# Optimization experiments

Measured on AMD Instinct MI355X. Metric: run time of the kernel, lower is better.

Reference implementation:

```python
import jax, jax.numpy as jnp
import numpy as np

HEAD_NUM = 8


def setup_inputs() -> dict:
    key = jax.random.key(0)
    ks = jax.random.split(key, 12)
    B, H, W, D = 8, 32, 32, 256
    Dh = D  # depth is even -> D_h = depth
    inner = Dh * HEAD_NUM
    s = 0.02
    inp = {
        "x": jax.random.normal(ks[0], (B, H, W, D), jnp.float32),
        "Kw": jax.random.normal(ks[1], (D, inner), jnp.float32) * s,
        "Kb": jnp.zeros((inner,), jnp.float32),
        "Qw": jax.random.normal(ks[2], (D, inner), jnp.float32) * s,
        "Qb": jnp.zeros((inner,), jnp.float32),
        "Vw": jax.random.normal(ks[3], (D, inner), jnp.float32) * s,
        "Vb": jnp.zeros((inner,), jnp.float32),
        "Pw": jax.random.normal(ks[4], (inner, D), jnp.float32) * s,
        "Pb": jnp.zeros((D,), jnp.float32),
        "row_tab": jax.random.normal(ks[5], (2 * H - 1, Dh // 2), jnp.float32) * s,
        "col_tab": jax.random.normal(ks[6], (2 * W - 1, Dh // 2), jnp.float32) * s,
    }
    return inp


def reference(x, Kw, Kb, Qw, Qb, Vw, Vb, Pw, Pb, row_tab, col_tab):
    B, H, W, D = x.shape
    hn = HEAD_NUM
    Dh = Kw.shape[1] // hn
    half = Dh // 2

    K = (x @ Kw + Kb).reshape(B, H, W, hn, Dh)
    Q = (x @ Qw + Qb).reshape(B, H, W, hn, Dh)
    V = (x @ Vw + Vb).reshape(B, H, W, hn, Dh)

    # content-content logits: [B,H,W,hn,H,W]
    score = jnp.einsum('bijhd,bklhd->bijhkl', Q, K)

    # relative row/col position bias via learned embeddings
    row_mat = jnp.arange(H)[None, :] - jnp.arange(H)[:, None] + H - 1  # (H,H)
    col_mat = jnp.arange(W)[:, None] - jnp.arange(W)[None, :] + W - 1  # (W,W)
    row_emb = row_tab[row_mat]  # (H,H,half)
    col_emb = col_tab[col_mat]  # (W,W,half)
    row_score = jnp.einsum('bijhd,ikd->bijhk', Q[..., :half], row_emb)[..., :, None]
    col_score = jnp.einsum('bijhd,jkd->bijhk', Q[..., half:], col_emb)[..., None, :]
    score = score + row_score + col_score

    attn = jax.nn.softmax(score.reshape(B, H, W, hn, H * W), axis=-1)
    attn = attn.reshape(B, H, W, hn, H, W)

    attended = jnp.einsum('bijhkl,bklhd->bijhd', attn, V).reshape(B, H, W, hn * Dh)
    return attended @ Pw + Pb
```

## Files before the change

kernel.cpp:

```cpp
#include <hip/hip_runtime.h>

typedef __attribute__((ext_vector_type(8))) short short8;
typedef __attribute__((ext_vector_type(4))) float f32x4;
typedef __attribute__((ext_vector_type(2))) unsigned int u32x2;
typedef __attribute__((ext_vector_type(4))) unsigned int u32x4;

__device__ __forceinline__ unsigned short f2bf(float f) {
  unsigned u = __float_as_uint(f);
  u += 0x7FFF + ((u >> 16) & 1);
  return (unsigned short)(u >> 16);
}
__device__ __forceinline__ unsigned packbf(float a, float b) {
  return (unsigned)f2bf(a) | ((unsigned)f2bf(b) << 16);
}
__device__ __forceinline__ float bf2f(unsigned short s) {
  return __uint_as_float(((unsigned)s) << 16);
}
__device__ __forceinline__ f32x4 mfma16(short8 a, short8 b, f32x4 c) {
  return __builtin_amdgcn_mfma_f32_16x16x32_bf16(a, b, c, 0, 0, 0);
}

typedef __attribute__((address_space(3))) unsigned int lds_u32;
typedef __attribute__((address_space(1))) const unsigned int glb_u32;
__device__ __forceinline__ void gll16(const void* g, void* l) {
  __builtin_amdgcn_global_load_lds((glb_u32*)g, (lds_u32*)l, 16, 0, 0);
}

__global__ void cvt_x_kernel(const float* __restrict__ in, unsigned short* __restrict__ out, int n) {
  int i = blockIdx.x * 256 + threadIdx.x;
  if (i < n) out[i] = f2bf(in[i]);
}

__global__ void transpose_cvt_kernel(const float* __restrict__ in, unsigned short* __restrict__ out,
                                     int K, int N) {
  int i = blockIdx.x * 256 + threadIdx.x;
  if (i < K * N) {
    int n = i / K, k = i - n * K;
    out[i] = f2bf(in[(size_t)k * N + n]);
  }
}

template<int MODE, int BMI>
__global__ __launch_bounds__(256, 2) void gemm128(const unsigned short* __restrict__ A,
    const unsigned short* __restrict__ BT, const float* __restrict__ bias,
    void* __restrict__ Cout, int Mdim, int Ndim, int Kdim) {
  constexpr int BM = 64 * BMI, MI = 2 * BMI;
  __shared__ short As[BM * 40];
  __shared__ short Bs[128 * 40];
  const int tid = threadIdx.x;
  const int wid = tid >> 6, lane = tid & 63;
  const int l15 = lane & 15, lg = lane >> 4;
  const int m0 = blockIdx.y * BM, n0 = blockIdx.x * 128;
  const int wr = (wid >> 1) * (BM / 2), wc = (wid & 1) * 64;
  const f32x4 z = {0.f, 0.f, 0.f, 0.f};
  f32x4 acc[MI][4];
#pragma unroll
  for (int mi = 0; mi < MI; ++mi)
#pragma unroll
    for (int ni = 0; ni < 4; ++ni) acc[mi][ni] = z;

  for (int kt = 0; kt < Kdim; kt += 32) {
#pragma unroll
    for (int it = 0; it < BMI; ++it) {
      int c = tid + it * 256;
      int row = c >> 2, c8 = (c & 3) * 8;
      *(short8*)&As[row * 40 + c8] = *(const short8*)(A + (size_t)(m0 + row) * Kdim + kt + c8);
    }
#pragma unroll
    for (int it = 0; it < 2; ++it) {
      int c = tid + it * 256;
      int row = c >> 2, c8 = (c & 3) * 8;
      *(short8*)&Bs[row * 40 + c8] = *(const short8*)(BT + (size_t)(n0 + row) * Kdim + kt + c8);
    }
    __syncthreads();
    short8 a[MI], b[4];
#pragma unroll
    for (int mi = 0; mi < MI; ++mi) a[mi] = *(const short8*)&As[(wr + mi * 16 + l15) * 40 + lg * 8];
#pragma unroll
    for (int ni = 0; ni < 4; ++ni) b[ni] = *(const short8*)&Bs[(wc + ni * 16 + l15) * 40 + lg * 8];
#pragma unroll
    for (int mi = 0; mi < MI; ++mi)
#pragma unroll
      for (int ni = 0; ni < 4; ++ni)
        acc[mi][ni] = mfma16(a[mi], b[ni], acc[mi][ni]);
    __syncthreads();
  }
#pragma unroll
  for (int mi = 0; mi < MI; ++mi)
#pragma unroll
    for (int ni = 0; ni < 4; ++ni)
#pragma unroll
      for (int e = 0; e < 4; ++e) {
        int gm = m0 + wr + mi * 16 + lg * 4 + e;
        int gn = n0 + wc + ni * 16 + l15;
        float v = acc[mi][ni][e] + bias[gn];
        if (MODE == 0) {
          ((unsigned short*)Cout)[(size_t)gm * Ndim + gn] = f2bf(v);
        } else if (MODE == 1) {
          ((float*)Cout)[(size_t)gm * Ndim + gn] = v;
        } else {
          int b_ = gm >> 10, pos = gm & 1023;
          int h = gn >> 8, d = gn & 255;
          ((unsigned short*)Cout)[((size_t)((b_ * 8 + h) * 256 + d)) * 1024 + pos] = f2bf(v);
        }
      }
}

__global__ __launch_bounds__(256, 4) void bias_mfma_kernel(const unsigned short* __restrict__ Q,
    const float* __restrict__ row_tab, const float* __restrict__ col_tab,
    float* __restrict__ Rb, float* __restrict__ Cb) {
  const int side = blockIdx.y >> 5;
  const int ij = blockIdx.y & 31;
  const int q4 = blockIdx.x;
  const int tid = threadIdx.x, wv = tid >> 6, lane = tid & 63;
  const int l15 = lane & 15, lg = lane >> 4;
  const float* tab = side ? col_tab : row_tab;
  const int doff = side ? 128 : 0;
  float* outp = side ? Cb : Rb;

  short8 eb[2][4];
#pragma unroll
  for (int nf = 0; nf < 2; ++nf) {
    int k = nf * 16 + l15;
    int trow = side ? (ij - k + 31) : (k - ij + 31);
    const float* tp = tab + (size_t)trow * 128 + lg * 8;
#pragma unroll
    for (int ks = 0; ks < 4; ++ks) {
      float4 f0 = *(const float4*)(tp + ks * 32);
      float4 f1 = *(const float4*)(tp + ks * 32 + 4);
      u32x4 r;
      r.x = packbf(f0.x, f0.y);
      r.y = packbf(f0.z, f0.w);
      r.z = packbf(f1.x, f1.y);
      r.w = packbf(f1.z, f1.w);
      eb[nf][ks] = *(short8*)&r;
    }
  }

  const f32x4 z = {0.f, 0.f, 0.f, 0.f};
  const int rbase = q4 * 512 + wv * 128;
#pragma unroll
  for (int mf = 0; mf < 8; ++mf) {
    int r = rbase + mf * 16 + l15;
    int b = r >> 8, jj = (r >> 3) & 31, h = r & 7;
    int q = side ? (jj * 32 + ij) : (ij * 32 + jj);
    const unsigned short* ap = Q + (size_t)(b * 1024 + q) * 2048 + h * 256 + doff + lg * 8;
    short8 af[4];
#pragma unroll
    for (int ks = 0; ks < 4; ++ks) af[ks] = *(const short8*)(ap + ks * 32);
    f32x4 a0 = z, a1 = z;
#pragma unroll
    for (int ks = 0; ks < 4; ++ks) {
      a0 = mfma16(af[ks], eb[0][ks], a0);
      a1 = mfma16(af[ks], eb[1][ks], a1);
    }
#pragma unroll
    for (int e = 0; e < 4; ++e) {
      int r2 = rbase + mf * 16 + lg * 4 + e;
      int b2 = r2 >> 8, jj2 = (r2 >> 3) & 31, h2 = r2 & 7;
      int q2 = side ? (jj2 * 32 + ij) : (ij * 32 + jj2);
      float* op = outp + ((size_t)((b2 * 8 + h2) * 1024 + q2)) * 32 + l15;
      op[0] = a0[e];
      op[16] = a1[e];
    }
  }
}

__global__ __launch_bounds__(512, 2) void attn_kernel(const unsigned short* __restrict__ Q,
    const unsigned short* __restrict__ K, const unsigned short* __restrict__ Vt,
    const float* __restrict__ Rb, const float* __restrict__ Cb,
    unsigned short* __restrict__ Att) {
  __shared__ __align__(16) char KV[4][32768];
  __shared__ unsigned short RbL[256 * 32];
  const int wgid = blockIdx.x;
  const int bh = (wgid & 7) * 8 + ((wgid >> 3) & 7);
  const int qblk = wgid >> 6;
  const int b = bh >> 3, h = bh & 7;
  const int tid = threadIdx.x, wv = tid >> 6, lane = tid & 63;
  const int l15 = lane & 15, lg = lane >> 4;
  const int q0w = qblk * 256 + wv * 32;

  const unsigned short* kbase = K + (size_t)(b * 1024) * 2048 + h * 256;
  const unsigned short* vbase = Vt + (size_t)bh * 256 * 1024;

  auto stage = [&](int buf, int t) {
#pragma unroll
    for (int it = 0; it < 2; ++it) {
      int s = it * 8192 + wv * 1024 + lane * 16;
      int key = s >> 9;
      int c = ((s >> 4) & 31) ^ (key & 7);
      gll16(kbase + (size_t)(t * 32 + key) * 2048 + c * 8, &KV[buf][it * 8192 + wv * 1024]);
    }
#pragma unroll
    for (int it = 0; it < 2; ++it) {
      int s = it * 8192 + wv * 1024 + lane * 16;
      int r = s >> 9;
      int cc = ((s >> 4) & 31) ^ (r & 7);
      int d = r * 8 + (cc >> 2);
      gll16(vbase + (size_t)d * 1024 + t * 32 + (cc & 3) * 8,
            &KV[buf][16384 + it * 8192 + wv * 1024]);
    }
  };

  stage(0, 0);
  stage(1, 1);

  short8 qa[2][8];
#pragma unroll
  for (int qf = 0; qf < 2; ++qf) {
    const unsigned short* qp = Q + (size_t)(b * 1024 + q0w + qf * 16 + l15) * 2048 + h * 256;
#pragma unroll
    for (int kk = 0; kk < 8; ++kk) qa[qf][kk] = *(const short8*)(qp + kk * 32 + lg * 8);
  }
  float4 cpre[2][2];
#pragma unroll
  for (int qf = 0; qf < 2; ++qf) {
    const float* cbp = Cb + ((size_t)bh * 1024 + q0w + qf * 16 + l15) * 32;
    cpre[qf][0] = *(const float4*)(cbp + lg * 4);
    cpre[qf][1] = *(const float4*)(cbp + 16 + lg * 4);
  }
  {
    const float* rsrc = Rb + ((size_t)bh * 1024 + qblk * 256) * 32;
#pragma unroll
    for (int i = 0; i < 16; ++i) {
      int idx = i * 512 + tid;
      RbL[idx] = f2bf(rsrc[idx]);
    }
  }
  asm volatile("s_waitcnt lgkmcnt(0)" ::: "memory");

  const f32x4 z = {0.f, 0.f, 0.f, 0.f};
  f32x4 o[16][2];
#pragma unroll
  for (int nf2 = 0; nf2 < 16; ++nf2) { o[nf2][0] = z; o[nf2][1] = z; }
  float m_r[2] = {-1e30f, -1e30f}, l_r[2] = {0.f, 0.f};

  const int nfd = lg >> 1;
  const int srcA = ((lg & 1) * 2) * 16 + l15, srcB = srcA + 16;
  const unsigned short* rbl0 = &RbL[(wv * 32 + l15) * 32];
  const unsigned short* rbl1 = rbl0 + 16 * 32;

  for (int t = 0; t < 32; ++t) {
    if (t < 30) stage((t + 2) & 3, t + 2);
    if (t < 30)       asm volatile("s_waitcnt vmcnt(8)" ::: "memory");
    else if (t == 30) asm volatile("s_waitcnt vmcnt(4)" ::: "memory");
    else              asm volatile("s_waitcnt vmcnt(0)" ::: "memory");
    __builtin_amdgcn_s_barrier();
    asm volatile("" ::: "memory");

    const char* kb = &KV[t & 3][0];
    const char* vb = &KV[t & 3][16384];

    f32x4 s[2][2] = {{z, z}, {z, z}};
#pragma unroll
    for (int kk = 0; kk < 8; ++kk) {
      int c0 = (kk * 4 + lg) ^ (l15 & 7);
      short8 k0 = *(const short8*)(kb + l15 * 512 + c0 * 16);
      int key1 = 16 + l15;
      int c1 = (kk * 4 + lg) ^ (key1 & 7);
      short8 k1 = *(const short8*)(kb + key1 * 512 + c1 * 16);
      s[0][0] = mfma16(k0, qa[0][kk], s[0][0]);
      s[1][0] = mfma16(k0, qa[1][kk], s[1][0]);
      s[0][1] = mfma16(k1, qa[0][kk], s[0][1]);
      s[1][1] = mfma16(k1, qa[1][kk], s[1][1]);
    }
    float rb0 = bf2f(rbl0[t]), rb1 = bf2f(rbl1[t]);
#pragma unroll
    for (int nf = 0; nf < 2; ++nf)
#pragma unroll
      for (int e = 0; e < 4; ++e) {
        s[0][nf][e] += rb0 + ((const float*)&cpre[0][nf])[e];
        s[1][nf][e] += rb1 + ((const float*)&cpre[1][nf])[e];
      }
    float tm[2];
#pragma unroll
    for (int qf = 0; qf < 2; ++qf) {
      float m2 = fmaxf(fmaxf(s[qf][0][0], s[qf][0][1]), fmaxf(s[qf][0][2], s[qf][0][3]));
#pragma unroll
      for (int e = 0; e < 4; ++e) m2 = fmaxf(m2, s[qf][1][e]);
      m2 = fmaxf(m2, __shfl_xor(m2, 16));
      m2 = fmaxf(m2, __shfl_xor(m2, 32));
      tm[qf] = m2;
    }
    if (__any((tm[0] > m_r[0] + 8.f) || (tm[1] > m_r[1] + 8.f))) {
#pragma unroll
      for (int qf = 0; qf < 2; ++qf) {
        float mn = fmaxf(m_r[qf], tm[qf]);
        float sc = __expf(m_r[qf] - mn);
        m_r[qf] = mn;
        l_r[qf] *= sc;
#pragma unroll
        for (int nf2 = 0; nf2 < 16; ++nf2)
#pragma unroll
          for (int e = 0; e < 4; ++e) o[nf2][qf][e] *= sc;
      }
    }
    short8 pb[2];
#pragma unroll
    for (int qf = 0; qf < 2; ++qf) {
      float ps = 0.f;
#pragma unroll
      for (int nf = 0; nf < 2; ++nf)
#pragma unroll
        for (int e = 0; e < 4; ++e) {
          float pv = __expf(s[qf][nf][e] - m_r[qf]);
          s[qf][nf][e] = pv;
          ps += pv;
        }
      ps += __shfl_xor(ps, 16);
      ps += __shfl_xor(ps, 32);
      l_r[qf] += ps;
      unsigned u0 = packbf(s[qf][0][0], s[qf][0][1]);
      unsigned u1 = packbf(s[qf][0][2], s[qf][0][3]);
      unsigned u2 = packbf(s[qf][1][0], s[qf][1][1]);
      unsigned u3 = packbf(s[qf][1][2], s[qf][1][3]);
      unsigned a0 = __shfl(u0, srcA), b0 = __shfl(u2, srcA);
      unsigned a1 = __shfl(u1, srcA), b1 = __shfl(u3, srcA);
      unsigned a2 = __shfl(u0, srcB), b2 = __shfl(u2, srcB);
      unsigned a3 = __shfl(u1, srcB), b3 = __shfl(u3, srcB);
      u32x4 r4;
      r4.x = nfd ? b0 : a0;
      r4.y = nfd ? b1 : a1;
      r4.z = nfd ? b2 : a2;
      r4.w = nfd ? b3 : a3;
      pb[qf] = *(short8*)&r4;
    }
#pragma unroll
    for (int nf2 = 0; nf2 < 16; ++nf2) {
      int d = nf2 * 16 + l15;
      int r = d >> 3;
      int cc = ((d & 7) * 4 + lg) ^ (r & 7);
      short8 vf = *(const short8*)(vb + r * 512 + cc * 16);
      o[nf2][0] = mfma16(vf, pb[0], o[nf2][0]);
      o[nf2][1] = mfma16(vf, pb[1], o[nf2][1]);
    }
  }
#pragma unroll
  for (int qf = 0; qf < 2; ++qf) {
    unsigned short* op = Att + (size_t)(b * 1024 + q0w + qf * 16 + l15) * 2048 + h * 256;
    float inv = 1.f / l_r[qf];
#pragma unroll
    for (int nf2 = 0; nf2 < 16; ++nf2) {
      u32x2 w;
      w.x = packbf(o[nf2][qf][0] * inv, o[nf2][qf][1] * inv);
      w.y = packbf(o[nf2][qf][2] * inv, o[nf2][qf][3] * inv);
      *(u32x2*)(op + nf2 * 16 + lg * 4) = w;
    }
  }
}

extern "C" void kernel_launch(void* const* d_in, const int* in_sizes, int n_in,
                              void* d_out, int out_size, void* d_ws, size_t ws_size,
                              hipStream_t stream) {
  (void)in_sizes; (void)n_in; (void)out_size;
  const float* x   = (const float*)d_in[0];
  const float* Kw  = (const float*)d_in[1];
  const float* Kb  = (const float*)d_in[2];
  const float* Qw  = (const float*)d_in[3];
  const float* Qb  = (const float*)d_in[4];
  const float* Vw  = (const float*)d_in[5];
  const float* Vb  = (const float*)d_in[6];
  const float* Pw  = (const float*)d_in[7];
  const float* Pb  = (const float*)d_in[8];
  const float* row_tab = (const float*)d_in[9];
  const float* col_tab = (const float*)d_in[10];
  float* out = (float*)d_out;

  char* ws = (char*)d_ws;
  size_t off = 0;
  auto alloc = [&](size_t bytes) { char* p = ws + off; off += bytes; return p; };
  unsigned short* Xb   = (unsigned short*)alloc((size_t)8192 * 256 * 2);
  unsigned short* WqT  = (unsigned short*)alloc((size_t)2048 * 256 * 2);
  unsigned short* WkT  = (unsigned short*)alloc((size_t)2048 * 256 * 2);
  unsigned short* WvT  = (unsigned short*)alloc((size_t)2048 * 256 * 2);
  unsigned short* PwT  = (unsigned short*)alloc((size_t)256 * 2048 * 2);
  unsigned short* Qg   = (unsigned short*)alloc((size_t)8192 * 2048 * 2);
  unsigned short* Kg   = (unsigned short*)alloc((size_t)8192 * 2048 * 2);
  unsigned short* VtG  = (unsigned short*)alloc((size_t)8192 * 2048 * 2);
  unsigned short* AttG = (unsigned short*)alloc((size_t)8192 * 2048 * 2);
  float* Rb = (float*)alloc((size_t)64 * 1024 * 32 * 4);
  float* Cb = (float*)alloc((size_t)64 * 1024 * 32 * 4);
  if (off > ws_size) return;

  cvt_x_kernel<<<8192, 256, 0, stream>>>(x, Xb, 8192 * 256);
  transpose_cvt_kernel<<<2048, 256, 0, stream>>>(Qw, WqT, 256, 2048);
  transpose_cvt_kernel<<<2048, 256, 0, stream>>>(Kw, WkT, 256, 2048);
  transpose_cvt_kernel<<<2048, 256, 0, stream>>>(Vw, WvT, 256, 2048);
  transpose_cvt_kernel<<<2048, 256, 0, stream>>>(Pw, PwT, 2048, 256);

  gemm128<0, 2><<<dim3(16, 64), 256, 0, stream>>>(Xb, WqT, Qb, Qg, 8192, 2048, 256);
  gemm128<0, 2><<<dim3(16, 64), 256, 0, stream>>>(Xb, WkT, Kb, Kg, 8192, 2048, 256);
  gemm128<2, 2><<<dim3(16, 64), 256, 0, stream>>>(Xb, WvT, Vb, VtG, 8192, 2048, 256);

  bias_mfma_kernel<<<dim3(4, 64), 256, 0, stream>>>(Qg, row_tab, col_tab, Rb, Cb);
  attn_kernel<<<256, 512, 0, stream>>>(Qg, Kg, VtG, Rb, Cb, AttG);
  gemm128<1, 1><<<dim3(2, 128), 256, 0, stream>>>(AttG, PwT, Pb, out, 8192, 256, 2048);
}
```

Before: 288.6 us.

## Halve attention workgroup size, double-buffer KV, compute softmax row sums via MFMA

The attention kernel now launches 512 workgroups of 256 threads, each covering 128 queries instead of 256, with a two-slot KV ring instead of four. A trailing barrier is added so a buffer is not overwritten while still being read. The softmax denominator is no longer reduced with shuffles; it is accumulated by an extra MFMA of a ones vector against the probability fragment. The RbL layout is transposed so each step reads a contiguous row. The goal is to raise occupancy and cut shuffle work, at the cost of a shallower prefetch pipeline, an extra barrier per step, and more redundant K/V loads across workgroups.

New measurement: 419.9 us. 1.46x slower.

```diff
diff --git a/kernel.cpp b/kernel.cpp
--- a/kernel.cpp
+++ b/kernel.cpp
@@ -166,44 +166,43 @@
   }
 }
 
-__global__ __launch_bounds__(512, 2) void attn_kernel(const unsigned short* __restrict__ Q,
+__global__ __launch_bounds__(256, 2) void attn_kernel(const unsigned short* __restrict__ Q,
     const unsigned short* __restrict__ K, const unsigned short* __restrict__ Vt,
     const float* __restrict__ Rb, const float* __restrict__ Cb,
     unsigned short* __restrict__ Att) {
-  __shared__ __align__(16) char KV[4][32768];
-  __shared__ unsigned short RbL[256 * 32];
+  __shared__ __align__(16) char KV[2][32768];
+  __shared__ unsigned short RbL[32 * 128];
   const int wgid = blockIdx.x;
   const int bh = (wgid & 7) * 8 + ((wgid >> 3) & 7);
   const int qblk = wgid >> 6;
   const int b = bh >> 3, h = bh & 7;
   const int tid = threadIdx.x, wv = tid >> 6, lane = tid & 63;
   const int l15 = lane & 15, lg = lane >> 4;
-  const int q0w = qblk * 256 + wv * 32;
+  const int q0w = qblk * 128 + wv * 32;
 
   const unsigned short* kbase = K + (size_t)(b * 1024) * 2048 + h * 256;
   const unsigned short* vbase = Vt + (size_t)bh * 256 * 1024;
 
   auto stage = [&](int buf, int t) {
 #pragma unroll
-    for (int it = 0; it < 2; ++it) {
-      int s = it * 8192 + wv * 1024 + lane * 16;
+    for (int it = 0; it < 4; ++it) {
+      int s = it * 4096 + wv * 1024 + lane * 16;
       int key = s >> 9;
       int c = ((s >> 4) & 31) ^ (key & 7);
-      gll16(kbase + (size_t)(t * 32 + key) * 2048 + c * 8, &KV[buf][it * 8192 + wv * 1024]);
-    }
-#pragma unroll
-    for (int it = 0; it < 2; ++it) {
-      int s = it * 8192 + wv * 1024 + lane * 16;
+      gll16(kbase + (size_t)(t * 32 + key) * 2048 + c * 8, &KV[buf][it * 4096 + wv * 1024]);
+    }
+#pragma unroll
+    for (int it = 0; it < 4; ++it) {
+      int s = it * 4096 + wv * 1024 + lane * 16;
       int r = s >> 9;
       int cc = ((s >> 4) & 31) ^ (r & 7);
       int d = r * 8 + (cc >> 2);
       gll16(vbase + (size_t)d * 1024 + t * 32 + (cc & 3) * 8,
-            &KV[buf][16384 + it * 8192 + wv * 1024]);
+            &KV[buf][16384 + it * 4096 + wv * 1024]);
     }
   };
 
   stage(0, 0);
-  stage(1, 1);
 
   short8 qa[2][8];
 #pragma unroll
@@ -220,11 +219,12 @@
     cpre[qf][1] = *(const float4*)(cbp + 16 + lg * 4);
   }
   {
-    const float* rsrc = Rb + ((size_t)bh * 1024 + qblk * 256) * 32;
+    const float* rsrc = Rb + ((size_t)bh * 1024 + qblk * 128) * 32;
 #pragma unroll
     for (int i = 0; i < 16; ++i) {
-      int idx = i * 512 + tid;
-      RbL[idx] = f2bf(rsrc[idx]);
+      int idx = i * 256 + tid;
+      int t = idx >> 7, q = idx & 127;
+      RbL[idx] = f2bf(rsrc[(size_t)q * 32 + t]);
     }
   }
   asm volatile("s_waitcnt lgkmcnt(0)" ::: "memory");
@@ -233,23 +233,24 @@
   f32x4 o[16][2];
 #pragma unroll
   for (int nf2 = 0; nf2 < 16; ++nf2) { o[nf2][0] = z; o[nf2][1] = z; }
-  float m_r[2] = {-1e30f, -1e30f}, l_r[2] = {0.f, 0.f};
+  f32x4 o_l[2] = {z, z};
+  float m_r[2] = {-1e30f, -1e30f};
 
   const int nfd = lg >> 1;
   const int srcA = ((lg & 1) * 2) * 16 + l15, srcB = srcA + 16;
-  const unsigned short* rbl0 = &RbL[(wv * 32 + l15) * 32];
-  const unsigned short* rbl1 = rbl0 + 16 * 32;
+  u32x4 onesu;
+  onesu.x = onesu.y = onesu.z = onesu.w = 0x3F803F80u;
+  const short8 ones = *(short8*)&onesu;
 
   for (int t = 0; t < 32; ++t) {
-    if (t < 30) stage((t + 2) & 3, t + 2);
-    if (t < 30)       asm volatile("s_waitcnt vmcnt(8)" ::: "memory");
-    else if (t == 30) asm volatile("s_waitcnt vmcnt(4)" ::: "memory");
-    else              asm volatile("s_waitcnt vmcnt(0)" ::: "memory");
+    if (t < 31) stage((t + 1) & 1, t + 1);
+    if (t < 31) asm volatile("s_waitcnt vmcnt(8)" ::: "memory");
+    else        asm volatile("s_waitcnt vmcnt(0)" ::: "memory");
     __builtin_amdgcn_s_barrier();
     asm volatile("" ::: "memory");
 
-    const char* kb = &KV[t & 3][0];
-    const char* vb = &KV[t & 3][16384];
+    const char* kb = &KV[t & 1][0];
+    const char* vb = &KV[t & 1][16384];
 
     f32x4 s[2][2] = {{z, z}, {z, z}};
 #pragma unroll
@@ -264,7 +265,8 @@
       s[0][1] = mfma16(k1, qa[0][kk], s[0][1]);
       s[1][1] = mfma16(k1, qa[1][kk], s[1][1]);
     }
-    float rb0 = bf2f(rbl0[t]), rb1 = bf2f(rbl1[t]);
+    float rb0 = bf2f(RbL[t * 128 + wv * 32 + l15]);
+    float rb1 = bf2f(RbL[t * 128 + wv * 32 + 16 + l15]);
 #pragma unroll
     for (int nf = 0; nf < 2; ++nf)
 #pragma unroll
@@ -288,7 +290,8 @@
         float mn = fmaxf(m_r[qf], tm[qf]);
         float sc = __expf(m_r[qf] - mn);
         m_r[qf] = mn;
-        l_r[qf] *= sc;
+#pragma unroll
+        for (int e = 0; e < 4; ++e) o_l[qf][e] *= sc;
 #pragma unroll
         for (int nf2 = 0; nf2 < 16; ++nf2)
 #pragma unroll
@@ -298,18 +301,11 @@
     short8 pb[2];
 #pragma unroll
     for (int qf = 0; qf < 2; ++qf) {
-      float ps = 0.f;
 #pragma unroll
       for (int nf = 0; nf < 2; ++nf)
 #pragma unroll
-        for (int e = 0; e < 4; ++e) {
-          float pv = __expf(s[qf][nf][e] - m_r[qf]);
-          s[qf][nf][e] = pv;
-          ps += pv;
-        }
-      ps += __shfl_xor(ps, 16);
-      ps += __shfl_xor(ps, 32);
-      l_r[qf] += ps;
+        for (int e = 0; e < 4; ++e)
+          s[qf][nf][e] = __expf(s[qf][nf][e] - m_r[qf]);
       unsigned u0 = packbf(s[qf][0][0], s[qf][0][1]);
       unsigned u1 = packbf(s[qf][0][2], s[qf][0][3]);
       unsigned u2 = packbf(s[qf][1][0], s[qf][1][1]);
@@ -325,6 +321,8 @@
       r4.w = nfd ? b3 : a3;
       pb[qf] = *(short8*)&r4;
     }
+    o_l[0] = mfma16(ones, pb[0], o_l[0]);
+    o_l[1] = mfma16(ones, pb[1], o_l[1]);
 #pragma unroll
     for (int nf2 = 0; nf2 < 16; ++nf2) {
       int d = nf2 * 16 + l15;
@@ -334,11 +332,13 @@
       o[nf2][0] = mfma16(vf, pb[0], o[nf2][0]);
       o[nf2][1] = mfma16(vf, pb[1], o[nf2][1]);
     }
+    asm volatile("" ::: "memory");
+    __builtin_amdgcn_s_barrier();
   }
 #pragma unroll
   for (int qf = 0; qf < 2; ++qf) {
     unsigned short* op = Att + (size_t)(b * 1024 + q0w + qf * 16 + l15) * 2048 + h * 256;
-    float inv = 1.f / l_r[qf];
+    float inv = 1.f / o_l[qf][0];
 #pragma unroll
     for (int nf2 = 0; nf2 < 16; ++nf2) {
       u32x2 w;
@@ -393,6 +393,6 @@
   gemm128<2, 2><<<dim3(16, 64), 256, 0, stream>>>(Xb, WvT, Vb, VtG, 8192, 2048, 256);
 
   bias_mfma_kernel<<<dim3(4, 64), 256, 0, stream>>>(Qg, row_tab, col_tab, Rb, Cb);
-  attn_kernel<<<256, 512, 0, stream>>>(Qg, Kg, VtG, Rb, Cb, AttG);
+  attn_kernel<<<512, 256, 0, stream>>>(Qg, Kg, VtG, Rb, Cb, AttG);
   gemm128<1, 1><<<dim3(2, 128), 256, 0, stream>>>(AttG, PwT, Pb, out, 8192, 256, 2048);
 }
```
